# Kernel optimization log

Measured on AMD Instinct MI355X. Metric: run time of the kernel, lower is better.

## Reference

```python
import jax, jax.numpy as jnp
import numpy as np

RPN_BBOX_STD_DEV = np.array([0.1, 0.1, 0.2, 0.2], dtype=np.float32)
PRE_NMS_LIMIT = 6000
PROPOSAL_COUNT = 1000
NMS_THRESHOLD = 0.7
BATCH = 8
NUM_ANCHORS = 261888


def setup_inputs() -> dict:
    key = jax.random.key(0)
    k1, k2, k3, k4 = jax.random.split(key, 4)
    fg = jax.random.uniform(k1, (BATCH, NUM_ANCHORS), dtype=jnp.float32)
    rpn_probs = jnp.stack([1.0 - fg, fg], axis=-1)  # [B, N, 2] (bg, fg)
    rpn_bbox = jax.random.normal(k2, (BATCH, NUM_ANCHORS, 4), dtype=jnp.float32) * 0.5
    # valid normalized anchors: y_min < y_max, x_min < x_max, inside [0, 1]
    mins = jax.random.uniform(k3, (BATCH, NUM_ANCHORS, 2), minval=0.0, maxval=0.85)
    size = jax.random.uniform(k4, (BATCH, NUM_ANCHORS, 2), minval=0.02, maxval=0.15)
    anchors = jnp.concatenate([mins, mins + size], axis=-1)  # [B, N, 4]
    return {"rpn_probs": rpn_probs, "rpn_bbox": rpn_bbox, "anchors": anchors}


def apply_box_deltas(boxes, deltas):
    # boxes: [..., (y1, x1, y2, x2)], deltas: [..., (dy, dx, log(dh), log(dw))]
    h = boxes[..., 2] - boxes[..., 0]
    w = boxes[..., 3] - boxes[..., 1]
    cy = boxes[..., 0] + 0.5 * h + deltas[..., 0] * h
    cx = boxes[..., 1] + 0.5 * w + deltas[..., 1] * w
    h = h * jnp.exp(deltas[..., 2])
    w = w * jnp.exp(deltas[..., 3])
    y1 = cy - 0.5 * h
    x1 = cx - 0.5 * w
    return jnp.stack([y1, x1, y1 + h, x1 + w], axis=-1)


def pairwise_iou(boxes):
    # boxes: [N, 4] -> iou [N, N]
    y1, x1, y2, x2 = boxes[:, 0], boxes[:, 1], boxes[:, 2], boxes[:, 3]
    area = (y2 - y1) * (x2 - x1)
    ih = jnp.maximum(jnp.minimum(y2[:, None], y2[None, :]) - jnp.maximum(y1[:, None], y1[None, :]), 0.0)
    iw = jnp.maximum(jnp.minimum(x2[:, None], x2[None, :]) - jnp.maximum(x1[:, None], x1[None, :]), 0.0)
    inter = ih * iw
    union = area[:, None] + area[None, :] - inter
    return jnp.where(union > 0.0, inter / union, 0.0)


def nms_single(boxes):
    # boxes: [K, 4], already sorted by score descending (top_k sorted=True).
    # Greedy NMS: a box is suppressed if it overlaps (IoU > thresh) a kept,
    # higher-scoring box. Sequential suppression via lax.scan over rows.
    K = boxes.shape[0]
    iou = pairwise_iou(boxes)  # [K, K]
    order = jnp.arange(K)

    def step(keep, i):
        suppress = keep[i] & (iou[i] > NMS_THRESHOLD) & (order > i)
        return keep & ~suppress, None

    keep, _ = jax.lax.scan(step, jnp.ones((K,), dtype=bool), order)
    # gather kept boxes in score order, pad with zeros to PROPOSAL_COUNT
    rank = jnp.cumsum(keep) - 1
    valid = keep & (rank < PROPOSAL_COUNT)
    dest = jnp.where(valid, rank, PROPOSAL_COUNT)  # invalid rows -> scratch row
    out = jnp.zeros((PROPOSAL_COUNT + 1, 4), boxes.dtype).at[dest].set(boxes)
    return out[:PROPOSAL_COUNT]


def reference(rpn_probs, rpn_bbox, anchors):
    scores = rpn_probs[:, :, 1]  # fg prob [B, N]
    deltas = rpn_bbox * jnp.asarray(RPN_BBOX_STD_DEV).reshape(1, 1, 4)
    k = min(PRE_NMS_LIMIT, anchors.shape[1])
    top_scores, idx = jax.lax.top_k(scores, k)  # sorted descending, [B, K]
    deltas_k = jnp.take_along_axis(deltas, idx[..., None], axis=1)   # [B, K, 4]
    anchors_k = jnp.take_along_axis(anchors, idx[..., None], axis=1)  # [B, K, 4]
    boxes = jnp.clip(apply_box_deltas(anchors_k, deltas_k), 0.0, 1.0)
    proposals = jax.vmap(nms_single)(boxes)  # [B, PROPOSAL_COUNT, 4]
    return proposals
```

## Files before the change

kernel.cpp:

```cpp
#include <hip/hip_runtime.h>
#include <hip/hip_bf16.h>

typedef unsigned long long ull;

constexpr int BATCH = 8;
constexpr int NA    = 261888;
constexpr int KSEL  = 6000;
constexpr int PROP  = 1000;
constexpr int CAP   = 8192;
constexpr int NBINS = 8192;
constexpr int HB    = 16;
constexpr int NBLK  = 94;
constexpr int NBLK0 = 48;
constexpr int SPLIT = 3072;
constexpr int MC0_W = 48;
constexpr int MC1_W = 46;
constexpr int MC0_SZ = SPLIT * MC0_W;
constexpr int MC1_SZ = (KSEL - SPLIT) * MC1_W;
constexpr int MBATCH = MC0_SZ + MC1_SZ;

constexpr size_t OFF_CNT   = 0;
constexpr size_t OFF_TSEL  = 512;
constexpr size_t OFF_KC    = 544;
constexpr size_t OFF_BOXES = 608;
constexpr size_t OFF_MASK  = 768608;
constexpr size_t OFF_DIAG  = OFF_MASK + 18057216;
constexpr size_t OFF_SUP   = OFF_DIAG + 385024;
constexpr size_t OFF_SKG   = OFF_SUP + 385024;
constexpr size_t OFF_GS    = OFF_SKG + 32768;
constexpr size_t OFF_KEYS  = OFF_MASK;
constexpr size_t OFF_HIST  = OFF_MASK + 2097152;

__device__ __forceinline__ int score_bin(float s) {
  int b = (int)(s * (float)NBINS);
  if (b < 0) b = 0;
  if (b > NBINS - 1) b = NBINS - 1;
  return b;
}

__global__ __launch_bounds__(256) void hist_kernel(const float4* __restrict__ probs4,
                                                   unsigned int* __restrict__ hist,
                                                   int* __restrict__ cnt,
                                                   ull* __restrict__ keys,
                                                   ull* __restrict__ gS) {
  __shared__ unsigned int lh[NBINS];
  for (int i = threadIdx.x; i < NBINS; i += 256) lh[i] = 0u;
  int fb = blockIdx.y * HB + blockIdx.x;
  if (threadIdx.x == 0) cnt[fb] = 0;
  {
    ull* kp = keys + (size_t)fb * 512;
    for (int i = threadIdx.x; i < 512; i += 256) kp[i] = ~0ull;
  }
  if (fb == 0) {
    for (int i = threadIdx.x; i < BATCH * NBLK; i += 256) gS[i] = 0ull;
  }
  __syncthreads();
  int b = blockIdx.y;
  const float4* p = probs4 + (size_t)b * (NA / 2);
  for (int a = blockIdx.x * 256 + threadIdx.x; a < NA / 2; a += HB * 256) {
    float4 v = p[a];
    atomicAdd(&lh[score_bin(v.y)], 1u);
    atomicAdd(&lh[score_bin(v.w)], 1u);
  }
  __syncthreads();
  unsigned int* gh = hist + ((size_t)b * HB + blockIdx.x) * NBINS;
  for (int i = threadIdx.x; i < NBINS; i += 256) gh[i] = lh[i];
}

__global__ __launch_bounds__(256) void thresh_kernel(const unsigned int* __restrict__ hist,
                                                     int* __restrict__ tsel) {
  constexpr int GR = NBINS / 256;
  __shared__ unsigned int ch[NBINS];
  __shared__ unsigned int gsum[256];
  int b = blockIdx.x;
  const unsigned int* h = hist + (size_t)b * HB * NBINS;
  for (int bin = threadIdx.x; bin < NBINS; bin += 256) {
    unsigned int s = 0;
    for (int k = 0; k < HB; ++k) s += h[(size_t)k * NBINS + bin];
    ch[bin] = s;
  }
  __syncthreads();
  unsigned int s = 0;
  int g0 = threadIdx.x * GR;
  for (int i = 0; i < GR; ++i) s += ch[g0 + i];
  gsum[threadIdx.x] = s;
  __syncthreads();
  if (threadIdx.x == 0) {
    unsigned int acc = 0;
    int g = 255;
    for (; g > 0; --g) {
      if (acc + gsum[g] >= (unsigned)KSEL) break;
      acc += gsum[g];
    }
    int t = g * GR;
    for (int bin = g * GR + GR - 1; bin >= g * GR; --bin) {
      acc += ch[bin];
      if (acc >= (unsigned)KSEL) { t = bin; break; }
    }
    tsel[b] = t;
  }
}

__global__ __launch_bounds__(256) void compact_kernel(const float4* __restrict__ probs4,
                                                      const int* __restrict__ tsel,
                                                      int* __restrict__ cnt,
                                                      ull* __restrict__ keys) {
  __shared__ int lcnt, lbase;
  __shared__ ull lbuf[2048];
  int b = blockIdx.y;
  int t = tsel[b];
  if (threadIdx.x == 0) lcnt = 0;
  __syncthreads();
  const float4* p = probs4 + (size_t)b * (NA / 2);
  for (int a = blockIdx.x * blockDim.x + threadIdx.x; a < NA / 2; a += gridDim.x * blockDim.x) {
    float4 v = p[a];
    if (score_bin(v.y) >= t) {
      int pos = atomicAdd(&lcnt, 1);
      unsigned int ib = ~__float_as_uint(v.y);
      lbuf[pos] = ((ull)ib << 32) | (unsigned int)(2 * a);
    }
    if (score_bin(v.w) >= t) {
      int pos = atomicAdd(&lcnt, 1);
      unsigned int ib = ~__float_as_uint(v.w);
      lbuf[pos] = ((ull)ib << 32) | (unsigned int)(2 * a + 1);
    }
  }
  __syncthreads();
  if (threadIdx.x == 0) lbase = atomicAdd(&cnt[b * 16], lcnt);
  __syncthreads();
  int n = lcnt, base = lbase;
  ull* kb = keys + (size_t)b * CAP;
  for (int i = threadIdx.x; i < n; i += 256) {
    int pos = base + i;
    if (pos < CAP) kb[pos] = lbuf[i];
  }
}

__global__ __launch_bounds__(256) void rankscatter_kernel(const float4* __restrict__ anchors4,
                                                          const float4* __restrict__ bbox4,
                                                          const int* __restrict__ cnt,
                                                          const ull* __restrict__ keys,
                                                          float4* __restrict__ boxes4) {
#pragma clang fp contract(off)
  __shared__ ull tile[1024];
  int b = blockIdx.y;
  int n = cnt[b * 16];
  if (n > CAP) n = CAP;
  int i = blockIdx.x * 256 + threadIdx.x;
  const ull* kb = keys + (size_t)b * CAP;
  ull my = (i < CAP) ? kb[(i < n) ? i : 0] : ~0ull;
  if (i >= n) my = ~0ull;
  unsigned int r = 0;
  int ntile = (n + 1023) & ~1023;
  for (int j0 = 0; j0 < ntile; j0 += 1024) {
    for (int k = threadIdx.x; k < 1024; k += 256) tile[k] = kb[j0 + k];
    __syncthreads();
#pragma unroll 16
    for (int k = 0; k < 1024; ++k) r += (tile[k] < my) ? 1u : 0u;
    __syncthreads();
  }
  if (i >= n || r >= (unsigned)KSEL) return;
  int a = (int)(unsigned int)(my & 0xffffffffull);
  float4 anc = anchors4[(size_t)b * NA + a];
  float4 d   = bbox4[(size_t)b * NA + a];
  float h = anc.z - anc.x;
  float w = anc.w - anc.y;
  float dy = d.x * 0.1f, dx = d.y * 0.1f, dh = d.z * 0.2f, dw = d.w * 0.2f;
  float cy = (anc.x + (0.5f * h)) + (dy * h);
  float cx = (anc.y + (0.5f * w)) + (dx * w);
  float h2 = h * expf(dh);
  float w2 = w * expf(dw);
  float y1 = cy - 0.5f * h2;
  float x1 = cx - 0.5f * w2;
  float y2 = y1 + h2;
  float x2 = x1 + w2;
  y1 = fminf(fmaxf(y1, 0.f), 1.f);
  x1 = fminf(fmaxf(x1, 0.f), 1.f);
  y2 = fminf(fmaxf(y2, 0.f), 1.f);
  x2 = fminf(fmaxf(x2, 0.f), 1.f);
  boxes4[(size_t)b * KSEL + r] = make_float4(y1, x1, y2, x2);
}

__global__ __launch_bounds__(256) void mask_kernel(const float4* __restrict__ boxes4,
                                                   ull* __restrict__ maskw,
                                                   ull* __restrict__ diagT,
                                                   ull* __restrict__ superT,
                                                   int rb2Base, int rowBase, int wordBase,
                                                   int wordLim, int stride, int chunkOff) {
#pragma clang fp contract(off)
  int cx = blockIdx.x, b = blockIdx.z;
  int rb2 = rb2Base + blockIdx.y;
  int w0 = 2 * rb2;
  int cb0 = w0 + 4 * cx;
  if (cb0 >= wordLim) return;
  __shared__ float4 colbox[4][64];
  __shared__ float  colca[4][64];
  __shared__ ull wtile[128][5];
  int tid = threadIdx.x, wv = tid >> 6, l = tid & 63;
  int cb = cb0 + wv;
  int rA = rb2 * 128 + l, rB = rA + 64;
  float4 zero = make_float4(0.f, 0.f, 0.f, 0.f);
  float4 boxA = (rA < KSEL) ? boxes4[(size_t)b * KSEL + rA] : zero;
  float4 boxB = (rB < KSEL) ? boxes4[(size_t)b * KSEL + rB] : zero;
  float areaA = (boxA.z - boxA.x) * (boxA.w - boxA.y);
  float areaB = (boxB.z - boxB.x) * (boxB.w - boxB.y);
  int c = cb * 64 + l;
  float4 cload = (cb < wordLim && c < KSEL) ? boxes4[(size_t)b * KSEL + c] : zero;
  colbox[wv][l] = cload;
  colca[wv][l] = (cload.z - cload.x) * (cload.w - cload.y);
  __syncthreads();
  ull bitsA = 0ull, bitsB = 0ull;
  if (cb < wordLim) {
#pragma unroll
    for (int u = 0; u < 64; ++u) {
      float4 cbx = colbox[wv][u];
      float ca = colca[wv][u];
      {
        float ih = fmaxf(fminf(boxA.z, cbx.z) - fmaxf(boxA.x, cbx.x), 0.f);
        float iw = fmaxf(fminf(boxA.w, cbx.w) - fmaxf(boxA.y, cbx.y), 0.f);
        float inter = ih * iw;
        float uni = (areaA + ca) - inter;
        float d = fmaf(-0.7f, uni, inter);
        float tt = 6e-7f * uni;
        bool keep;
        if (__builtin_fabsf(d) <= tt) keep = (inter / uni) > 0.7f;
        else keep = d > 0.f;
        if (keep) bitsA |= (1ull << u);
      }
      {
        float ih = fmaxf(fminf(boxB.z, cbx.z) - fmaxf(boxB.x, cbx.x), 0.f);
        float iw = fmaxf(fminf(boxB.w, cbx.w) - fmaxf(boxB.y, cbx.y), 0.f);
        float inter = ih * iw;
        float uni = (areaB + ca) - inter;
        float d = fmaf(-0.7f, uni, inter);
        float tt = 6e-7f * uni;
        bool keep;
        if (__builtin_fabsf(d) <= tt) keep = (inter / uni) > 0.7f;
        else keep = d > 0.f;
        if (keep) bitsB |= (1ull << u);
      }
    }
    if (cb == w0) {
      bitsA &= (l == 63) ? 0ull : (~0ull << (l + 1));
      ull colT = 0ull;
#pragma unroll
      for (int k = 0; k < 64; ++k) {
        ull bk = __ballot(((bitsA >> k) & 1ull) != 0ull);
        if (l == k) colT = bk;
      }
      diagT[((size_t)b * NBLK + w0) * 64 + l] = colT;
    }
    if (cb == w0 + 1) {
      superT[((size_t)b * NBLK + w0) * 64 + l] = bitsA;
      bitsB &= (l == 63) ? 0ull : (~0ull << (l + 1));
      ull colT = 0ull;
#pragma unroll
      for (int k = 0; k < 64; ++k) {
        ull bk = __ballot(((bitsB >> k) & 1ull) != 0ull);
        if (l == k) colT = bk;
      }
      diagT[((size_t)b * NBLK + w0 + 1) * 64 + l] = colT;
    }
    if (cb == w0 + 2) {
      superT[((size_t)b * NBLK + w0 + 1) * 64 + l] = bitsB;
    }
  }
  wtile[l][wv] = bitsA;
  wtile[l + 64][wv] = bitsB;
  __syncthreads();
  int base_row = rb2 * 128;
#pragma unroll
  for (int pass = 0; pass < 2; ++pass) {
    int idx = pass * 256 + tid;
    int rr = idx >> 2, w = idx & 3;
    int row = base_row + rr;
    int cw = cb0 + w;
    if (row < KSEL && cw < wordLim)
      maskw[(size_t)b * MBATCH + chunkOff + (size_t)(row - rowBase) * stride + (cw - wordBase)]
        = wtile[rr][w];
  }
}

__global__ __launch_bounds__(64) void maskx_kernel(const float4* __restrict__ boxes4,
                                                   const int* __restrict__ skeepG,
                                                   const int* __restrict__ kc,
                                                   ull* __restrict__ gS) {
#pragma clang fp contract(off)
  __shared__ float4 colbox[64];
  __shared__ float  colca[64];
  int b = blockIdx.z;
  int kept0 = kc[b * 2];
  int rg = blockIdx.y;
  if (rg * 64 >= kept0) return;
  int l = threadIdx.x;
  int w = NBLK0 + blockIdx.x;
  int c = w * 64 + l;
  float4 zero = make_float4(0.f, 0.f, 0.f, 0.f);
  float4 cld = (c < KSEL) ? boxes4[(size_t)b * KSEL + c] : zero;
  colbox[l] = cld;
  colca[l] = (cld.z - cld.x) * (cld.w - cld.y);
  __syncthreads();
  int idx = rg * 64 + l;
  ull bits = 0ull;
  if (idx < kept0) {
    int r = skeepG[b * 1024 + idx];
    float4 rb = boxes4[(size_t)b * KSEL + r];
    float rA = (rb.z - rb.x) * (rb.w - rb.y);
#pragma unroll
    for (int u = 0; u < 64; ++u) {
      float4 cbx = colbox[u];
      float ca = colca[u];
      float ih = fmaxf(fminf(rb.z, cbx.z) - fmaxf(rb.x, cbx.x), 0.f);
      float iw = fmaxf(fminf(rb.w, cbx.w) - fmaxf(rb.y, cbx.y), 0.f);
      float inter = ih * iw;
      float uni = (rA + ca) - inter;
      float d = fmaf(-0.7f, uni, inter);
      float tt = 6e-7f * uni;
      bool keep;
      if (__builtin_fabsf(d) <= tt) keep = (inter / uni) > 0.7f;
      else keep = d > 0.f;
      if (keep) bits |= (1ull << u);
    }
  }
  unsigned lo = (unsigned)bits, hi = (unsigned)(bits >> 32);
#pragma unroll
  for (int m = 1; m < 64; m <<= 1) {
    lo |= (unsigned)__shfl_xor((int)lo, m, 64);
    hi |= (unsigned)__shfl_xor((int)hi, m, 64);
  }
  if (l == 0) {
    ull v = (ull)lo | ((ull)hi << 32);
    if (v) atomicOr(&gS[b * NBLK + w], v);
  }
}

template<int PHASE>
__global__ __launch_bounds__(256, 1) void scan_kernel(const float4* __restrict__ boxes4,
                                                      const ull* __restrict__ maskw,
                                                      const ull* __restrict__ diagT,
                                                      const ull* __restrict__ superT,
                                                      int* __restrict__ skeepG,
                                                      int* __restrict__ kc,
                                                      const ull* __restrict__ gS,
                                                      float4* __restrict__ out4) {
  __shared__ ull ldiagT[NBLK0 * 64];
  __shared__ ull lsuper[NBLK0 * 64];
  __shared__ ull S[96];
  __shared__ ull S_urg;
  __shared__ int klist[2][64];
  __shared__ int skeep[1024];
  __shared__ int s_kept, s_done, s_klen[2];
  int b = blockIdx.x;
  int tid = threadIdx.x;
  int lane = tid & 63;
  const ull* mb = maskw + (size_t)b * MBATCH;
  const int nB = PHASE ? NBLK0 : 0;
  const int nE = PHASE ? NBLK : NBLK0;

  const ull* dt = diagT + (size_t)b * NBLK * 64;
  const ull* st = superT + (size_t)b * NBLK * 64;
  for (int i = nB * 64 + tid; i < nE * 64; i += 256) {
    ldiagT[i - nB * 64] = dt[i];
    lsuper[i - nB * 64] = st[i];
  }
  if (PHASE == 0) {
    if (tid < 96) S[tid] = 0ull;
    if (tid == 0) { s_kept = 0; s_done = 0; s_klen[0] = 0; s_klen[1] = 0; S_urg = 0ull; }
  } else {
    int k0 = kc[b * 2], d0 = kc[b * 2 + 1];
    if (tid < 96) S[tid] = (tid >= NBLK0 && tid < NBLK) ? gS[b * NBLK + tid] : 0ull;
    for (int i = tid; i < k0; i += 256) skeep[i] = skeepG[b * 1024 + i];
    if (tid == 0) { s_kept = k0; s_done = d0; s_klen[0] = 0; s_klen[1] = 0; S_urg = 0ull; }
  }
  __syncthreads();

  for (int n = nB; n < nE; ++n) {
    if (s_done) break;
    if (tid < 64) {
      ull Sn = S[n] | S_urg;
      int i0 = n * 64;
      ull colT = ldiagT[i0 - nB * 64 + lane];
      ull sd = (n + 1 < NBLK) ? lsuper[i0 - nB * 64 + lane] : 0ull;
      int nval = KSEL - i0;
      ull valid = (nval >= 64) ? ~0ull : ((1ull << nval) - 1ull);
      ull A = ~Sn & valid;
      ull K = 0ull;
      int kept = s_kept;
      int done = 0;
      while (A) {
        int u = __builtin_ctzll(A);
        ++kept;
        K |= (1ull << u);
        if (kept >= PROP) { done = 1; break; }
        ull sup = __ballot(((colT >> u) & 1ull) != 0ull);
        A &= ~(sup | (1ull << u));
      }
      int klen = __builtin_popcountll(K);
      int kbase = kept - klen;
      if ((K >> lane) & 1ull) {
        int rank = __builtin_popcountll(K & ((1ull << lane) - 1ull));
        skeep[kbase + rank] = i0 + lane;
        klist[n & 1][rank] = i0 + lane;
      }
      int klp = (klen + 3) & ~3;
      if (klen > 0 && lane >= klen && lane < klp)
        klist[n & 1][lane] = i0 + __builtin_ctzll(K);
      unsigned ulo = (unsigned)sd, uhi = (unsigned)(sd >> 32);
      if (!((K >> lane) & 1ull)) { ulo = 0u; uhi = 0u; }
#pragma unroll
      for (int m = 1; m < 64; m <<= 1) {
        ulo |= (unsigned)__shfl_xor((int)ulo, m, 64);
        uhi |= (unsigned)__shfl_xor((int)uhi, m, 64);
      }
      if (lane == 0) {
        s_klen[n & 1] = klen;
        S_urg = (ull)ulo | ((ull)uhi << 32);
        s_kept = kept;
        if (done) s_done = 1;
      }
    } else {
      int prev = (n & 1) ^ 1;
      int kl = s_klen[prev];
      int lt = tid - 64;
      int wi = lt >> 2;
      int sub = lt & 3;
      int w = n + 1 + wi;
      if (kl > 0 && w < nE) {
        const int* kp = klist[prev];
        int klp4 = (kl + 3) & ~3;
        int per = klp4 >> 2;
        int base = sub * per;
        ull acc = 0ull;
#pragma unroll 8
        for (int ri = 0; ri < per; ++ri) {
          int r = kp[base + ri];
          size_t addr = (PHASE == 0) ? ((size_t)r * MC0_W + w)
                                     : ((size_t)MC0_SZ + (size_t)(r - SPLIT) * MC1_W + (w - NBLK0));
          acc |= mb[addr];
        }
        if (acc) atomicOr(&S[w], acc);
      }
    }
    __syncthreads();
  }

  if (PHASE == 0) {
    int k0 = s_kept;
    if (k0 > PROP) k0 = PROP;
    for (int i = tid; i < k0; i += 256) skeepG[b * 1024 + i] = skeep[i];
    if (tid == 0) { kc[b * 2] = k0; kc[b * 2 + 1] = s_done; }
  } else {
    int fin = s_kept;
    if (fin > PROP) fin = PROP;
    const float4* bx = boxes4 + (size_t)b * KSEL;
    for (int r2 = tid; r2 < PROP; r2 += 256) {
      float4 v = make_float4(0.f, 0.f, 0.f, 0.f);
      if (r2 < fin) v = bx[skeep[r2]];
      out4[(size_t)b * PROP + r2] = v;
    }
  }
}

extern "C" void kernel_launch(void* const* d_in, const int* in_sizes, int n_in,
                              void* d_out, int out_size, void* d_ws, size_t ws_size,
                              hipStream_t stream) {
  const float4* probs4  = (const float4*)d_in[0];
  const float4* bbox4   = (const float4*)d_in[1];
  const float4* anchors4= (const float4*)d_in[2];
  float4* out4 = (float4*)d_out;
  char* ws = (char*)d_ws;

  int* cnt           = (int*)(ws + OFF_CNT);
  int* tsel          = (int*)(ws + OFF_TSEL);
  int* kc            = (int*)(ws + OFF_KC);
  float4* boxes4     = (float4*)(ws + OFF_BOXES);
  ull* maskw         = (ull*)(ws + OFF_MASK);
  ull* diagT         = (ull*)(ws + OFF_DIAG);
  ull* superT        = (ull*)(ws + OFF_SUP);
  int* skeepG        = (int*)(ws + OFF_SKG);
  ull* gS            = (ull*)(ws + OFF_GS);
  ull* keys          = (ull*)(ws + OFF_KEYS);
  unsigned int* hist = (unsigned int*)(ws + OFF_HIST);

  hipLaunchKernelGGL(hist_kernel,        dim3(HB, BATCH),    dim3(256), 0, stream, probs4, hist, cnt, keys, gS);
  hipLaunchKernelGGL(thresh_kernel,      dim3(BATCH),        dim3(256), 0, stream, hist, tsel);
  hipLaunchKernelGGL(compact_kernel,     dim3(128, BATCH),   dim3(256), 0, stream, probs4, tsel, cnt, keys);
  hipLaunchKernelGGL(rankscatter_kernel, dim3(32, BATCH),    dim3(256), 0, stream, anchors4, bbox4, cnt, keys, boxes4);
  hipLaunchKernelGGL(mask_kernel, dim3(12, 24, BATCH), dim3(256), 0, stream,
                     boxes4, maskw, diagT, superT, 0, 0, 0, NBLK0, MC0_W, 0);
  hipLaunchKernelGGL(mask_kernel, dim3(12, 23, BATCH), dim3(256), 0, stream,
                     boxes4, maskw, diagT, superT, 24, SPLIT, NBLK0, NBLK, MC1_W, MC0_SZ);
  scan_kernel<0><<<dim3(BATCH), dim3(256), 0, stream>>>(boxes4, maskw, diagT, superT,
                                                        skeepG, kc, gS, out4);
  hipLaunchKernelGGL(maskx_kernel, dim3(NBLK - NBLK0, 16, BATCH), dim3(64), 0, stream,
                     boxes4, skeepG, kc, gS);
  scan_kernel<1><<<dim3(BATCH), dim3(256), 0, stream>>>(boxes4, maskw, diagT, superT,
                                                        skeepG, kc, gS, out4);
}
```

Before: 319.0 us.

## Process two 64-box NMS words per scan step to halve block barriers

The sequential NMS scan now resolves 128 boxes per iteration instead of 64. The mask kernel emits three diagonal transposed tiles and four super-diagonal tiles per 128-row block, so the leader wave can resolve both words and carry urgent suppression into the next two words. This halves the number of __syncthreads-separated iterations on the serial critical path. In exchange it adds more ballots, shuffles and shared memory per step, and the bulk OR workers lag by a larger window.

```diff
diff --git a/kernel.cpp b/kernel.cpp
--- a/kernel.cpp
+++ b/kernel.cpp
@@ -18,6 +18,8 @@
 constexpr int MC0_SZ = SPLIT * MC0_W;
 constexpr int MC1_SZ = (KSEL - SPLIT) * MC1_W;
 constexpr int MBATCH = MC0_SZ + MC1_SZ;
+constexpr int NB128  = 47;
+constexpr int M0     = 24;
 
 constexpr size_t OFF_CNT   = 0;
 constexpr size_t OFF_TSEL  = 512;
@@ -25,8 +27,8 @@
 constexpr size_t OFF_BOXES = 608;
 constexpr size_t OFF_MASK  = 768608;
 constexpr size_t OFF_DIAG  = OFF_MASK + 18057216;
-constexpr size_t OFF_SUP   = OFF_DIAG + 385024;
-constexpr size_t OFF_SKG   = OFF_SUP + 385024;
+constexpr size_t OFF_SUP   = OFF_DIAG + 577536;
+constexpr size_t OFF_SKG   = OFF_SUP + 770048;
 constexpr size_t OFF_GS    = OFF_SKG + 32768;
 constexpr size_t OFF_KEYS  = OFF_MASK;
 constexpr size_t OFF_HIST  = OFF_MASK + 2097152;
@@ -240,7 +242,11 @@
         if (keep) bitsB |= (1ull << u);
       }
     }
-    if (cb == w0) {
+  }
+  if (cx == 0) {
+    size_t dbase = ((size_t)b * NB128 + rb2) * 3 * 64;
+    size_t sbase = ((size_t)b * NB128 + rb2) * 4 * 64;
+    if (wv == 0) {
       bitsA &= (l == 63) ? 0ull : (~0ull << (l + 1));
       ull colT = 0ull;
 #pragma unroll
@@ -248,21 +254,32 @@
         ull bk = __ballot(((bitsA >> k) & 1ull) != 0ull);
         if (l == k) colT = bk;
       }
-      diagT[((size_t)b * NBLK + w0) * 64 + l] = colT;
-    }
-    if (cb == w0 + 1) {
-      superT[((size_t)b * NBLK + w0) * 64 + l] = bitsA;
+      diagT[dbase + 0 * 64 + l] = colT;
+    }
+    if (wv == 1) {
+      ull colT = 0ull;
+#pragma unroll
+      for (int k = 0; k < 64; ++k) {
+        ull bk = __ballot(((bitsA >> k) & 1ull) != 0ull);
+        if (l == k) colT = bk;
+      }
+      diagT[dbase + 1 * 64 + l] = colT;
       bitsB &= (l == 63) ? 0ull : (~0ull << (l + 1));
-      ull colT = 0ull;
+      ull colT2 = 0ull;
 #pragma unroll
       for (int k = 0; k < 64; ++k) {
         ull bk = __ballot(((bitsB >> k) & 1ull) != 0ull);
-        if (l == k) colT = bk;
-      }
-      diagT[((size_t)b * NBLK + w0 + 1) * 64 + l] = colT;
-    }
-    if (cb == w0 + 2) {
-      superT[((size_t)b * NBLK + w0 + 1) * 64 + l] = bitsB;
+        if (l == k) colT2 = bk;
+      }
+      diagT[dbase + 2 * 64 + l] = colT2;
+    }
+    if (wv == 2) {
+      superT[sbase + 0 * 64 + l] = bitsA;
+      superT[sbase + 1 * 64 + l] = bitsB;
+    }
+    if (wv == 3) {
+      superT[sbase + 2 * 64 + l] = bitsA;
+      superT[sbase + 3 * 64 + l] = bitsB;
     }
   }
   wtile[l][wv] = bitsA;
@@ -343,97 +360,133 @@
                                                       int* __restrict__ kc,
                                                       const ull* __restrict__ gS,
                                                       float4* __restrict__ out4) {
-  __shared__ ull ldiagT[NBLK0 * 64];
-  __shared__ ull lsuper[NBLK0 * 64];
+  __shared__ ull ldiag[M0 * 3 * 64];
+  __shared__ ull lsup[M0 * 4 * 64];
   __shared__ ull S[96];
-  __shared__ ull S_urg;
-  __shared__ int klist[2][64];
+  __shared__ ull S_urgA, S_urgB;
+  __shared__ int klist[2][128];
   __shared__ int skeep[1024];
   __shared__ int s_kept, s_done, s_klen[2];
   int b = blockIdx.x;
   int tid = threadIdx.x;
   int lane = tid & 63;
   const ull* mb = maskw + (size_t)b * MBATCH;
-  const int nB = PHASE ? NBLK0 : 0;
-  const int nE = PHASE ? NBLK : NBLK0;
-
-  const ull* dt = diagT + (size_t)b * NBLK * 64;
-  const ull* st = superT + (size_t)b * NBLK * 64;
-  for (int i = nB * 64 + tid; i < nE * 64; i += 256) {
-    ldiagT[i - nB * 64] = dt[i];
-    lsuper[i - nB * 64] = st[i];
+  const int mB = PHASE ? M0 : 0;
+  const int mE = PHASE ? NB128 : M0;
+  const int wE = PHASE ? NBLK : NBLK0;
+
+  {
+    const ull* dt = diagT + ((size_t)b * NB128 + mB) * 3 * 64;
+    int cntd = (mE - mB) * 3 * 64;
+    for (int i = tid; i < cntd; i += 256) ldiag[i] = dt[i];
+    const ull* st = superT + ((size_t)b * NB128 + mB) * 4 * 64;
+    int cnts = (mE - mB) * 4 * 64;
+    for (int i = tid; i < cnts; i += 256) lsup[i] = st[i];
   }
   if (PHASE == 0) {
     if (tid < 96) S[tid] = 0ull;
-    if (tid == 0) { s_kept = 0; s_done = 0; s_klen[0] = 0; s_klen[1] = 0; S_urg = 0ull; }
+    if (tid == 0) { s_kept = 0; s_done = 0; s_klen[0] = 0; s_klen[1] = 0; S_urgA = 0ull; S_urgB = 0ull; }
   } else {
     int k0 = kc[b * 2], d0 = kc[b * 2 + 1];
     if (tid < 96) S[tid] = (tid >= NBLK0 && tid < NBLK) ? gS[b * NBLK + tid] : 0ull;
     for (int i = tid; i < k0; i += 256) skeep[i] = skeepG[b * 1024 + i];
-    if (tid == 0) { s_kept = k0; s_done = d0; s_klen[0] = 0; s_klen[1] = 0; S_urg = 0ull; }
-  }
-  __syncthreads();
-
-  for (int n = nB; n < nE; ++n) {
+    if (tid == 0) { s_kept = k0; s_done = d0; s_klen[0] = 0; s_klen[1] = 0; S_urgA = 0ull; S_urgB = 0ull; }
+  }
+  __syncthreads();
+
+  for (int m = mB; m < mE; ++m) {
     if (s_done) break;
     if (tid < 64) {
-      ull Sn = S[n] | S_urg;
-      int i0 = n * 64;
-      ull colT = ldiagT[i0 - nB * 64 + lane];
-      ull sd = (n + 1 < NBLK) ? lsuper[i0 - nB * 64 + lane] : 0ull;
-      int nval = KSEL - i0;
-      ull valid = (nval >= 64) ? ~0ull : ((1ull << nval) - 1ull);
-      ull A = ~Sn & valid;
-      ull K = 0ull;
+      int lm = m - mB;
+      ull Sn0 = S[2 * m] | S_urgA;
+      ull Sn1 = S[2 * m + 1] | S_urgB;
+      ull cA0 = ldiag[(lm * 3 + 0) * 64 + lane];
+      ull cB0 = ldiag[(lm * 3 + 1) * 64 + lane];
+      ull cB1 = ldiag[(lm * 3 + 2) * 64 + lane];
+      ull sA2 = lsup[(lm * 4 + 0) * 64 + lane];
+      ull sB2 = lsup[(lm * 4 + 1) * 64 + lane];
+      ull sA3 = lsup[(lm * 4 + 2) * 64 + lane];
+      ull sB3 = lsup[(lm * 4 + 3) * 64 + lane];
+      int base = m * 128;
+      int nval = KSEL - base;
+      ull valid0 = (nval >= 64) ? ~0ull : ((nval <= 0) ? 0ull : ((1ull << nval) - 1ull));
+      int nv1 = nval - 64;
+      ull valid1 = (nv1 >= 64) ? ~0ull : ((nv1 <= 0) ? 0ull : ((1ull << nv1) - 1ull));
+      ull A0 = ~Sn0 & valid0;
+      ull A1 = ~Sn1 & valid1;
+      ull K0 = 0ull, K1 = 0ull;
       int kept = s_kept;
       int done = 0;
-      while (A) {
-        int u = __builtin_ctzll(A);
+      while (A0 | A1) {
+        bool lo = (A0 != 0ull);
+        int u = lo ? __builtin_ctzll(A0) : __builtin_ctzll(A1);
         ++kept;
-        K |= (1ull << u);
+        if (lo) K0 |= (1ull << u); else K1 |= (1ull << u);
         if (kept >= PROP) { done = 1; break; }
-        ull sup = __ballot(((colT >> u) & 1ull) != 0ull);
-        A &= ~(sup | (1ull << u));
-      }
-      int klen = __builtin_popcountll(K);
+        if (lo) {
+          ull sup0 = __ballot(((cA0 >> u) & 1ull) != 0ull);
+          ull sup1 = __ballot(((cB0 >> u) & 1ull) != 0ull);
+          A0 &= ~(sup0 | (1ull << u));
+          A1 &= ~sup1;
+        } else {
+          ull sup1 = __ballot(((cB1 >> u) & 1ull) != 0ull);
+          A1 &= ~(sup1 | (1ull << u));
+        }
+      }
+      int klen0 = __builtin_popcountll(K0);
+      int klen  = klen0 + __builtin_popcountll(K1);
       int kbase = kept - klen;
-      if ((K >> lane) & 1ull) {
-        int rank = __builtin_popcountll(K & ((1ull << lane) - 1ull));
-        skeep[kbase + rank] = i0 + lane;
-        klist[n & 1][rank] = i0 + lane;
+      if ((K0 >> lane) & 1ull) {
+        int rank = __builtin_popcountll(K0 & ((1ull << lane) - 1ull));
+        skeep[kbase + rank] = base + lane;
+        klist[m & 1][rank] = base + lane;
+      }
+      if ((K1 >> lane) & 1ull) {
+        int rank = klen0 + __builtin_popcountll(K1 & ((1ull << lane) - 1ull));
+        skeep[kbase + rank] = base + 64 + lane;
+        klist[m & 1][rank] = base + 64 + lane;
       }
       int klp = (klen + 3) & ~3;
-      if (klen > 0 && lane >= klen && lane < klp)
-        klist[n & 1][lane] = i0 + __builtin_ctzll(K);
-      unsigned ulo = (unsigned)sd, uhi = (unsigned)(sd >> 32);
-      if (!((K >> lane) & 1ull)) { ulo = 0u; uhi = 0u; }
-#pragma unroll
-      for (int m = 1; m < 64; m <<= 1) {
-        ulo |= (unsigned)__shfl_xor((int)ulo, m, 64);
-        uhi |= (unsigned)__shfl_xor((int)uhi, m, 64);
+      int padn = klp - klen;
+      if (klen > 0 && lane < padn) {
+        int fk = base + ((K0 != 0ull) ? __builtin_ctzll(K0) : (64 + __builtin_ctzll(K1)));
+        klist[m & 1][klen + lane] = fk;
+      }
+      ull ua2 = 0ull, ua3 = 0ull;
+      if ((K0 >> lane) & 1ull) { ua2 |= sA2; ua3 |= sA3; }
+      if ((K1 >> lane) & 1ull) { ua2 |= sB2; ua3 |= sB3; }
+      unsigned a2lo = (unsigned)ua2, a2hi = (unsigned)(ua2 >> 32);
+      unsigned a3lo = (unsigned)ua3, a3hi = (unsigned)(ua3 >> 32);
+#pragma unroll
+      for (int mm = 1; mm < 64; mm <<= 1) {
+        a2lo |= (unsigned)__shfl_xor((int)a2lo, mm, 64);
+        a2hi |= (unsigned)__shfl_xor((int)a2hi, mm, 64);
+        a3lo |= (unsigned)__shfl_xor((int)a3lo, mm, 64);
+        a3hi |= (unsigned)__shfl_xor((int)a3hi, mm, 64);
       }
       if (lane == 0) {
-        s_klen[n & 1] = klen;
-        S_urg = (ull)ulo | ((ull)uhi << 32);
+        s_klen[m & 1] = klen;
+        S_urgA = (ull)a2lo | ((ull)a2hi << 32);
+        S_urgB = (ull)a3lo | ((ull)a3hi << 32);
         s_kept = kept;
         if (done) s_done = 1;
       }
     } else {
-      int prev = (n & 1) ^ 1;
+      int prev = (m & 1) ^ 1;
       int kl = s_klen[prev];
       int lt = tid - 64;
       int wi = lt >> 2;
       int sub = lt & 3;
-      int w = n + 1 + wi;
-      if (kl > 0 && w < nE) {
+      int w = 2 * m + 2 + wi;
+      if (kl > 0 && w < wE) {
         const int* kp = klist[prev];
         int klp4 = (kl + 3) & ~3;
         int per = klp4 >> 2;
-        int base = sub * per;
+        int bs = sub * per;
         ull acc = 0ull;
 #pragma unroll 8
         for (int ri = 0; ri < per; ++ri) {
-          int r = kp[base + ri];
+          int r = kp[bs + ri];
           size_t addr = (PHASE == 0) ? ((size_t)r * MC0_W + w)
                                      : ((size_t)MC0_SZ + (size_t)(r - SPLIT) * MC1_W + (w - NBLK0));
           acc |= mb[addr];
```

Measured after the change: 375.3 us. +17.7%, slower.

## Overlap phase-0 NMS scan with second-half mask construction in one launch

Applied to the files above, without the earlier changes.

Merges the second mask-building launch and the phase-0 scan into a single grid. The first 8 blocks run the sequential scan over the first half of the candidates while the remaining blocks compute the IoU bitmask for the second half. The intent is to hide the latency-bound single-block-per-batch scan behind parallel mask work and to drop one launch. The fused kernel carries launch_bounds(256,1) and the union of both bodies' shared memory, which may lower occupancy for the mask blocks. It also assumes the scan blocks get scheduled early.

```diff
diff --git a/kernel.cpp b/kernel.cpp
--- a/kernel.cpp
+++ b/kernel.cpp
@@ -181,21 +181,20 @@
   boxes4[(size_t)b * KSEL + r] = make_float4(y1, x1, y2, x2);
 }
 
-__global__ __launch_bounds__(256) void mask_kernel(const float4* __restrict__ boxes4,
-                                                   ull* __restrict__ maskw,
-                                                   ull* __restrict__ diagT,
-                                                   ull* __restrict__ superT,
-                                                   int rb2Base, int rowBase, int wordBase,
-                                                   int wordLim, int stride, int chunkOff) {
+__device__ __forceinline__ void mask_body(const float4* __restrict__ boxes4,
+                                          ull* __restrict__ maskw,
+                                          ull* __restrict__ diagT,
+                                          ull* __restrict__ superT,
+                                          int cx, int rb2, int b,
+                                          int rowBase, int wordBase,
+                                          int wordLim, int stride, int chunkOff) {
 #pragma clang fp contract(off)
-  int cx = blockIdx.x, b = blockIdx.z;
-  int rb2 = rb2Base + blockIdx.y;
+  __shared__ float4 colbox[4][64];
+  __shared__ float  colca[4][64];
+  __shared__ ull wtile[128][5];
   int w0 = 2 * rb2;
   int cb0 = w0 + 4 * cx;
   if (cb0 >= wordLim) return;
-  __shared__ float4 colbox[4][64];
-  __shared__ float  colca[4][64];
-  __shared__ ull wtile[128][5];
   int tid = threadIdx.x, wv = tid >> 6, l = tid & 63;
   int cb = cb0 + wv;
   int rA = rb2 * 128 + l, rB = rA + 64;
@@ -281,68 +280,16 @@
   }
 }
 
-__global__ __launch_bounds__(64) void maskx_kernel(const float4* __restrict__ boxes4,
-                                                   const int* __restrict__ skeepG,
-                                                   const int* __restrict__ kc,
-                                                   ull* __restrict__ gS) {
-#pragma clang fp contract(off)
-  __shared__ float4 colbox[64];
-  __shared__ float  colca[64];
-  int b = blockIdx.z;
-  int kept0 = kc[b * 2];
-  int rg = blockIdx.y;
-  if (rg * 64 >= kept0) return;
-  int l = threadIdx.x;
-  int w = NBLK0 + blockIdx.x;
-  int c = w * 64 + l;
-  float4 zero = make_float4(0.f, 0.f, 0.f, 0.f);
-  float4 cld = (c < KSEL) ? boxes4[(size_t)b * KSEL + c] : zero;
-  colbox[l] = cld;
-  colca[l] = (cld.z - cld.x) * (cld.w - cld.y);
-  __syncthreads();
-  int idx = rg * 64 + l;
-  ull bits = 0ull;
-  if (idx < kept0) {
-    int r = skeepG[b * 1024 + idx];
-    float4 rb = boxes4[(size_t)b * KSEL + r];
-    float rA = (rb.z - rb.x) * (rb.w - rb.y);
-#pragma unroll
-    for (int u = 0; u < 64; ++u) {
-      float4 cbx = colbox[u];
-      float ca = colca[u];
-      float ih = fmaxf(fminf(rb.z, cbx.z) - fmaxf(rb.x, cbx.x), 0.f);
-      float iw = fmaxf(fminf(rb.w, cbx.w) - fmaxf(rb.y, cbx.y), 0.f);
-      float inter = ih * iw;
-      float uni = (rA + ca) - inter;
-      float d = fmaf(-0.7f, uni, inter);
-      float tt = 6e-7f * uni;
-      bool keep;
-      if (__builtin_fabsf(d) <= tt) keep = (inter / uni) > 0.7f;
-      else keep = d > 0.f;
-      if (keep) bits |= (1ull << u);
-    }
-  }
-  unsigned lo = (unsigned)bits, hi = (unsigned)(bits >> 32);
-#pragma unroll
-  for (int m = 1; m < 64; m <<= 1) {
-    lo |= (unsigned)__shfl_xor((int)lo, m, 64);
-    hi |= (unsigned)__shfl_xor((int)hi, m, 64);
-  }
-  if (l == 0) {
-    ull v = (ull)lo | ((ull)hi << 32);
-    if (v) atomicOr(&gS[b * NBLK + w], v);
-  }
-}
-
 template<int PHASE>
-__global__ __launch_bounds__(256, 1) void scan_kernel(const float4* __restrict__ boxes4,
-                                                      const ull* __restrict__ maskw,
-                                                      const ull* __restrict__ diagT,
-                                                      const ull* __restrict__ superT,
-                                                      int* __restrict__ skeepG,
-                                                      int* __restrict__ kc,
-                                                      const ull* __restrict__ gS,
-                                                      float4* __restrict__ out4) {
+__device__ __forceinline__ void scan_body(const float4* __restrict__ boxes4,
+                                          const ull* __restrict__ maskw,
+                                          const ull* __restrict__ diagT,
+                                          const ull* __restrict__ superT,
+                                          int* __restrict__ skeepG,
+                                          int* __restrict__ kc,
+                                          const ull* __restrict__ gS,
+                                          float4* __restrict__ out4,
+                                          int b) {
   __shared__ ull ldiagT[NBLK0 * 64];
   __shared__ ull lsuper[NBLK0 * 64];
   __shared__ ull S[96];
@@ -350,7 +297,6 @@
   __shared__ int klist[2][64];
   __shared__ int skeep[1024];
   __shared__ int s_kept, s_done, s_klen[2];
-  int b = blockIdx.x;
   int tid = threadIdx.x;
   int lane = tid & 63;
   const ull* mb = maskw + (size_t)b * MBATCH;
@@ -461,6 +407,99 @@
   }
 }
 
+__global__ __launch_bounds__(256) void mask0_kernel(const float4* __restrict__ boxes4,
+                                                    ull* __restrict__ maskw,
+                                                    ull* __restrict__ diagT,
+                                                    ull* __restrict__ superT) {
+  mask_body(boxes4, maskw, diagT, superT,
+            blockIdx.x, blockIdx.y, blockIdx.z, 0, 0, NBLK0, MC0_W, 0);
+}
+
+__global__ __launch_bounds__(256, 1) void fused0_kernel(const float4* __restrict__ boxes4,
+                                                        ull* __restrict__ maskw,
+                                                        ull* __restrict__ diagT,
+                                                        ull* __restrict__ superT,
+                                                        int* __restrict__ skeepG,
+                                                        int* __restrict__ kc,
+                                                        const ull* __restrict__ gS,
+                                                        float4* __restrict__ out4) {
+  if (blockIdx.x < 8) {
+    scan_body<0>(boxes4, maskw, diagT, superT, skeepG, kc, gS, out4, blockIdx.x);
+  } else {
+    int idx = blockIdx.x - 8;
+    int cx = idx % 12;
+    int tmp = idx / 12;
+    int rb2 = 24 + (tmp % 23);
+    int b = tmp / 23;
+    mask_body(boxes4, maskw, diagT, superT,
+              cx, rb2, b, SPLIT, NBLK0, NBLK, MC1_W, MC0_SZ);
+  }
+}
+
+__global__ __launch_bounds__(64) void maskx_kernel(const float4* __restrict__ boxes4,
+                                                   const int* __restrict__ skeepG,
+                                                   const int* __restrict__ kc,
+                                                   ull* __restrict__ gS) {
+#pragma clang fp contract(off)
+  __shared__ float4 colbox[64];
+  __shared__ float  colca[64];
+  int b = blockIdx.z;
+  int kept0 = kc[b * 2];
+  int rg = blockIdx.y;
+  if (rg * 64 >= kept0) return;
+  int l = threadIdx.x;
+  int w = NBLK0 + blockIdx.x;
+  int c = w * 64 + l;
+  float4 zero = make_float4(0.f, 0.f, 0.f, 0.f);
+  float4 cld = (c < KSEL) ? boxes4[(size_t)b * KSEL + c] : zero;
+  colbox[l] = cld;
+  colca[l] = (cld.z - cld.x) * (cld.w - cld.y);
+  __syncthreads();
+  int idx = rg * 64 + l;
+  ull bits = 0ull;
+  if (idx < kept0) {
+    int r = skeepG[b * 1024 + idx];
+    float4 rb = boxes4[(size_t)b * KSEL + r];
+    float rA = (rb.z - rb.x) * (rb.w - rb.y);
+#pragma unroll
+    for (int u = 0; u < 64; ++u) {
+      float4 cbx = colbox[u];
+      float ca = colca[u];
+      float ih = fmaxf(fminf(rb.z, cbx.z) - fmaxf(rb.x, cbx.x), 0.f);
+      float iw = fmaxf(fminf(rb.w, cbx.w) - fmaxf(rb.y, cbx.y), 0.f);
+      float inter = ih * iw;
+      float uni = (rA + ca) - inter;
+      float d = fmaf(-0.7f, uni, inter);
+      float tt = 6e-7f * uni;
+      bool keep;
+      if (__builtin_fabsf(d) <= tt) keep = (inter / uni) > 0.7f;
+      else keep = d > 0.f;
+      if (keep) bits |= (1ull << u);
+    }
+  }
+  unsigned lo = (unsigned)bits, hi = (unsigned)(bits >> 32);
+#pragma unroll
+  for (int m = 1; m < 64; m <<= 1) {
+    lo |= (unsigned)__shfl_xor((int)lo, m, 64);
+    hi |= (unsigned)__shfl_xor((int)hi, m, 64);
+  }
+  if (l == 0) {
+    ull v = (ull)lo | ((ull)hi << 32);
+    if (v) atomicOr(&gS[b * NBLK + w], v);
+  }
+}
+
+__global__ __launch_bounds__(256, 1) void scan1_kernel(const float4* __restrict__ boxes4,
+                                                       const ull* __restrict__ maskw,
+                                                       const ull* __restrict__ diagT,
+                                                       const ull* __restrict__ superT,
+                                                       int* __restrict__ skeepG,
+                                                       int* __restrict__ kc,
+                                                       const ull* __restrict__ gS,
+                                                       float4* __restrict__ out4) {
+  scan_body<1>(boxes4, maskw, diagT, superT, skeepG, kc, gS, out4, blockIdx.x);
+}
+
 extern "C" void kernel_launch(void* const* d_in, const int* in_sizes, int n_in,
                               void* d_out, int out_size, void* d_ws, size_t ws_size,
                               hipStream_t stream) {
@@ -486,14 +525,12 @@
   hipLaunchKernelGGL(thresh_kernel,      dim3(BATCH),        dim3(256), 0, stream, hist, tsel);
   hipLaunchKernelGGL(compact_kernel,     dim3(128, BATCH),   dim3(256), 0, stream, probs4, tsel, cnt, keys);
   hipLaunchKernelGGL(rankscatter_kernel, dim3(32, BATCH),    dim3(256), 0, stream, anchors4, bbox4, cnt, keys, boxes4);
-  hipLaunchKernelGGL(mask_kernel, dim3(12, 24, BATCH), dim3(256), 0, stream,
-                     boxes4, maskw, diagT, superT, 0, 0, 0, NBLK0, MC0_W, 0);
-  hipLaunchKernelGGL(mask_kernel, dim3(12, 23, BATCH), dim3(256), 0, stream,
-                     boxes4, maskw, diagT, superT, 24, SPLIT, NBLK0, NBLK, MC1_W, MC0_SZ);
-  scan_kernel<0><<<dim3(BATCH), dim3(256), 0, stream>>>(boxes4, maskw, diagT, superT,
-                                                        skeepG, kc, gS, out4);
+  hipLaunchKernelGGL(mask0_kernel, dim3(12, 24, BATCH), dim3(256), 0, stream,
+                     boxes4, maskw, diagT, superT);
+  hipLaunchKernelGGL(fused0_kernel, dim3(8 + 12 * 23 * BATCH), dim3(256), 0, stream,
+                     boxes4, maskw, diagT, superT, skeepG, kc, gS, out4);
   hipLaunchKernelGGL(maskx_kernel, dim3(NBLK - NBLK0, 16, BATCH), dim3(64), 0, stream,
                      boxes4, skeepG, kc, gS);
-  scan_kernel<1><<<dim3(BATCH), dim3(256), 0, stream>>>(boxes4, maskw, diagT, superT,
-                                                        skeepG, kc, gS, out4);
-}
+  hipLaunchKernelGGL(scan1_kernel, dim3(BATCH), dim3(256), 0, stream,
+                     boxes4, maskw, diagT, superT, skeepG, kc, gS, out4);
+}
```

New measurement: 282.5 us. 1.13x faster.
